# Performance work log

Measured on AMD Instinct MI355X. Metric: run time of the kernel, lower is better.

Reference implementation:

```python
import jax, jax.numpy as jnp
import numpy as np

N = 100000   # nodes
E = 1600000  # edges (avg degree 16)
D = 128      # feature / hidden dim
C = 64       # classes
L = 4        # number of GCNII layers
ALPHA = 0.1
LAMDA = 0.5


def setup_inputs() -> dict:
    key = jax.random.key(0)
    ks = jax.random.split(key, 8)
    stdv = 1.0 / np.sqrt(D)
    x = jax.random.normal(ks[0], (N, D), jnp.float32)
    edge_src = jax.random.randint(ks[1], (E,), 0, N)
    edge_dst = jax.random.randint(ks[2], (E,), 0, N)
    edge_weight = jax.random.uniform(ks[3], (E,), jnp.float32)
    w_in = jax.random.uniform(ks[4], (D, D), jnp.float32, -stdv, stdv)
    b_in = jnp.zeros((D,), jnp.float32)
    gcn_w = jax.random.uniform(ks[5], (L, D, D), jnp.float32, -stdv, stdv)
    w_out = jax.random.uniform(ks[6], (D, C), jnp.float32, -stdv, stdv)
    b_out = jnp.zeros((C,), jnp.float32)
    return {"x": x, "edge_src": edge_src, "edge_dst": edge_dst,
            "edge_weight": edge_weight, "w_in": w_in, "b_in": b_in,
            "gcn_w": gcn_w, "w_out": w_out, "b_out": b_out}


def _spmm(edge_src, edge_dst, edge_weight, h):
    # torch.sparse.mm(adj, h): out[i] = sum_j adj[i,j] * h[j]
    # row = dst, col = src in COO terms.
    return jax.ops.segment_sum(edge_weight[:, None] * h[edge_src],
                               edge_dst, num_segments=N)


def reference(x, edge_src, edge_dst, edge_weight, w_in, b_in, gcn_w, w_out, b_out):
    h0 = jax.nn.relu(x @ w_in + b_in)          # [N, D] initial residual
    h = h0
    for l in range(L):
        # GCNConvII called with l_arg = l+1 -> theta = log(lamda/(l_arg+1) + 1)
        theta = float(np.log(LAMDA / (l + 2) + 1.0))
        hi = _spmm(edge_src, edge_dst, edge_weight, h)      # sparse SpMM
        support = (1.0 - ALPHA) * hi + ALPHA * h0           # initial-residual mix
        out = theta * (support @ gcn_w[l]) + (1.0 - theta) * support
        out = out + h                                       # identity residual
        h = jax.nn.relu(out)
    logits = h @ w_out + b_out                              # [N, C]
    return jax.nn.log_softmax(logits, axis=1)
```

## Files before the change

### kernel.cpp

```cpp
#include <hip/hip_runtime.h>
#include <hip/hip_fp16.h>
#include <math.h>

#define N_NODES 100000
#define N_EDGES 1600000
#define DIM     128
#define NCLS    64
#define ALPHA   0.1f

#define NB      391
#define CAP     5120
#define NF      ((size_t)N_NODES * DIM)
#define STRIPES (N_NODES / 16)
#define CHUNK   4096

typedef __attribute__((ext_vector_type(8))) _Float16 f16x8;
typedef __attribute__((ext_vector_type(4))) float    f32x4;

__device__ __forceinline__ __half2 u2h2(unsigned int u) {
    union { unsigned int u; __half2 h; } x; x.u = u; return x.h;
}
__device__ __forceinline__ unsigned int h22u(__half2 h) {
    union { unsigned int u; __half2 h; } x; x.h = h; return x.u;
}


__global__ __launch_bounds__(256) void k_part(const int* __restrict__ src,
                                              const int* __restrict__ dst,
                                              const float* __restrict__ ew,
                                              int* __restrict__ bucket_cursor,
                                              int2* __restrict__ ebuf) {
    __shared__ int lhist[NB], gbase[NB];
    int t = threadIdx.x;
    for (int b = t; b < NB; b += 256) lhist[b] = 0;
    __syncthreads();
    int base = blockIdx.x * CHUNK;
    int end = min(base + CHUNK, N_EDGES);
    for (int i = base + t; i < end; i += 256)
        atomicAdd(&lhist[dst[i] >> 8], 1);
    __syncthreads();
    for (int b = t; b < NB; b += 256) {
        int c = lhist[b];
        gbase[b] = c ? atomicAdd(&bucket_cursor[b], c) : 0;
        lhist[b] = 0;
    }
    __syncthreads();
    for (int i = base + t; i < end; i += 256) {
        int d = dst[i];
        int b = d >> 8;
        int r = atomicAdd(&lhist[b], 1);
        ebuf[(size_t)b * CAP + gbase[b] + r] =
            make_int2(src[i] | ((d & 255) << 17),
                      __float_as_int((1.0f - ALPHA) * ew[i]));
    }
}

__global__ __launch_bounds__(256) void k_sortbucket(
    const int2* __restrict__ ebuf, const int* __restrict__ bucket_cursor,
    int2* __restrict__ rowspan, int2* __restrict__ colw) {
    __shared__ int cnt[256], pref[256], lcur[256];
    int t = threadIdx.x, b = blockIdx.x;
    cnt[t] = 0;
    __syncthreads();
    int beg = b * CAP, end = beg + bucket_cursor[b];
    for (int i = beg + t; i < end; i += 256)
        atomicAdd(&cnt[ebuf[i].x >> 17], 1);
    __syncthreads();
    int v = cnt[t];
    pref[t] = v;
    __syncthreads();
    for (int off = 1; off < 256; off <<= 1) {
        int u = (t >= off) ? pref[t - off] : 0;
        __syncthreads();
        pref[t] += u;
        __syncthreads();
    }
    int excl = pref[t] - v;
    int node = b * 256 + t;
    if (node < N_NODES) rowspan[node] = make_int2(beg + excl, beg + excl + v);
    lcur[t] = beg + excl;
    __syncthreads();
    for (int i = beg + t; i < end; i += 256) {
        int2 e = ebuf[i];
        int pos = atomicAdd(&lcur[e.x >> 17], 1);
        unsigned int w2 = h22u(__float2half2_rn(__int_as_float(e.y)));
        colw[pos] = make_int2(e.x & 0x1FFFF, (int)w2);
    }
}

__global__ void k_prepw(const float* __restrict__ gcnw, const float* __restrict__ wout,
                        const float* __restrict__ win, unsigned short* __restrict__ wp,
                        int* __restrict__ bucket_cursor) {
    int tid = blockIdx.x * 256 + threadIdx.x;
    if (tid < NB) bucket_cursor[tid] = 0;
    if (tid < 65536) {
        int l = tid >> 14;
        int r = tid & 16383;
        int j = r & 7, lane = (r >> 3) & 63, ch = (r >> 9) & 3, nt = r >> 11;
        int n = nt * 16 + (lane & 15);
        int k = ch * 32 + (lane >> 4) * 8 + j;
        float theta = logf(0.5f / (float)(l + 2) + 1.0f);
        float v = theta * gcnw[l * 16384 + k * 128 + n] + ((k == n) ? (1.f - theta) : 0.f);
        wp[tid] = __half_as_ushort(__float2half(v));
    } else if (tid < 73728) {
        int r = tid - 65536;
        int j = r & 7, lane = (r >> 3) & 63, ch = (r >> 9) & 3, nt = r >> 11;
        int n = nt * 16 + (lane & 15);
        int k = ch * 32 + (lane >> 4) * 8 + j;
        wp[tid] = __half_as_ushort(__float2half(wout[k * 64 + n]));
    } else if (tid < 90112) {
        int r = tid - 73728;
        int j = r & 7, lane = (r >> 3) & 63, ch = (r >> 9) & 3, nt = r >> 11;
        int n = nt * 16 + (lane & 15);
        int k = ch * 32 + (lane >> 4) * 8 + j;
        wp[tid] = __half_as_ushort(__float2half(win[k * 128 + n]));
    }
}

__device__ __forceinline__ void gather_tile(
    const int2* __restrict__ rowspan, const int2* __restrict__ colw,
    const unsigned short* __restrict__ h, const unsigned short* __restrict__ h0,
    unsigned short* sup, int r0, int wave, int slot, int seg) {
    __half2 z2 = __float2half2_rn(0.f);
    __half2 al2 = __float2half2_rn(ALPHA);
    for (int i = 0; i < 4; i++) {
        int n_loc = wave * 4 + i;
        int node = r0 + n_loc;
        int2 span = rowspan[node];
        int beg = span.x, end = span.y;

        __half2 acc2[4] = {z2, z2, z2, z2};
        if (slot == 0) {
            uint4 z = *(const uint4*)(h0 + (size_t)node * DIM + seg * 8);
            acc2[0] = __hmul2(al2, u2h2(z.x));
            acc2[1] = __hmul2(al2, u2h2(z.y));
            acc2[2] = __hmul2(al2, u2h2(z.z));
            acc2[3] = __hmul2(al2, u2h2(z.w));
        }

        int last = end - 1;
        for (int e = beg; e < end; e += 16) {
            int e0 = e + slot, e1 = e0 + 4, e2 = e0 + 8, e3 = e0 + 12;
            int2 c0 = colw[min(e0, last)];
            int2 c1 = colw[min(e1, last)];
            int2 c2 = colw[min(e2, last)];
            int2 c3 = colw[min(e3, last)];
            uint4 r0v = *(const uint4*)(h + (size_t)c0.x * DIM + seg * 8);
            uint4 r1v = *(const uint4*)(h + (size_t)c1.x * DIM + seg * 8);
            uint4 r2v = *(const uint4*)(h + (size_t)c2.x * DIM + seg * 8);
            uint4 r3v = *(const uint4*)(h + (size_t)c3.x * DIM + seg * 8);
            __half2 w0 = (e0 < end) ? u2h2((unsigned int)c0.y) : z2;
            __half2 w1 = (e1 < end) ? u2h2((unsigned int)c1.y) : z2;
            __half2 w2 = (e2 < end) ? u2h2((unsigned int)c2.y) : z2;
            __half2 w3 = (e3 < end) ? u2h2((unsigned int)c3.y) : z2;
            acc2[0] = __hfma2(w0, u2h2(r0v.x), acc2[0]);
            acc2[1] = __hfma2(w0, u2h2(r0v.y), acc2[1]);
            acc2[2] = __hfma2(w0, u2h2(r0v.z), acc2[2]);
            acc2[3] = __hfma2(w0, u2h2(r0v.w), acc2[3]);
            acc2[0] = __hfma2(w1, u2h2(r1v.x), acc2[0]);
            acc2[1] = __hfma2(w1, u2h2(r1v.y), acc2[1]);
            acc2[2] = __hfma2(w1, u2h2(r1v.z), acc2[2]);
            acc2[3] = __hfma2(w1, u2h2(r1v.w), acc2[3]);
            acc2[0] = __hfma2(w2, u2h2(r2v.x), acc2[0]);
            acc2[1] = __hfma2(w2, u2h2(r2v.y), acc2[1]);
            acc2[2] = __hfma2(w2, u2h2(r2v.z), acc2[2]);
            acc2[3] = __hfma2(w2, u2h2(r2v.w), acc2[3]);
            acc2[0] = __hfma2(w3, u2h2(r3v.x), acc2[0]);
            acc2[1] = __hfma2(w3, u2h2(r3v.y), acc2[1]);
            acc2[2] = __hfma2(w3, u2h2(r3v.z), acc2[2]);
            acc2[3] = __hfma2(w3, u2h2(r3v.w), acc2[3]);
        }

        #pragma unroll
        for (int j = 0; j < 4; j++) {
            unsigned int u = __shfl_xor(h22u(acc2[j]), 16);
            acc2[j] = __hadd2(acc2[j], u2h2(u));
            u = __shfl_xor(h22u(acc2[j]), 32);
            acc2[j] = __hadd2(acc2[j], u2h2(u));
        }

        if (slot == 0) {
            int g = seg ^ n_loc;
            *(uint4*)(sup + n_loc * 128 + g * 8) =
                make_uint4(h22u(acc2[0]), h22u(acc2[1]), h22u(acc2[2]), h22u(acc2[3]));
        }
    }
}

__global__ __launch_bounds__(256, 6) void k_layer_fused(
    const int2* __restrict__ rowspan, const int2* __restrict__ colw,
    const unsigned short* __restrict__ h,
    const unsigned short* __restrict__ h0,
    const unsigned short* __restrict__ wp,
    unsigned short* __restrict__ hout) {
    __shared__ unsigned short sup[16 * 128];
    int wave = threadIdx.x >> 6, lane = threadIdx.x & 63;
    int slot = lane >> 4, seg = lane & 15;
    int r0 = blockIdx.x * 16;

    gather_tile(rowspan, colw, h, h0, sup, r0, wave, slot, seg);
    __syncthreads();

    int m = lane & 15, q = lane >> 4;
    f32x4 acc[2];
    acc[0] = (f32x4){0.f, 0.f, 0.f, 0.f};
    acc[1] = (f32x4){0.f, 0.f, 0.f, 0.f};
    #pragma unroll
    for (int ch = 0; ch < 4; ch++) {
        int g = (4 * ch + q) ^ m;
        f16x8 a = *(const f16x8*)(sup + m * 128 + g * 8);
        #pragma unroll
        for (int t2 = 0; t2 < 2; t2++) {
            int nt = wave * 2 + t2;
            f16x8 b = *(const f16x8*)(wp + (((nt * 4 + ch) * 64 + lane) << 3));
            acc[t2] = __builtin_amdgcn_mfma_f32_16x16x32_f16(a, b, acc[t2], 0, 0, 0);
        }
    }
    #pragma unroll
    for (int t2 = 0; t2 < 2; t2++) {
        int col = (wave * 2 + t2) * 16 + m;
        #pragma unroll
        for (int r = 0; r < 4; r++) {
            int row = r0 + q * 4 + r;
            size_t idx = (size_t)row * DIM + col;
            float hp = __half2float(__ushort_as_half(h[idx]));
            float o = acc[t2][r] + hp;
            hout[idx] = __half_as_ushort(__float2half(fmaxf(o, 0.f)));
        }
    }
}

__global__ __launch_bounds__(256, 6) void k_layer_fused_out(
    const int2* __restrict__ rowspan, const int2* __restrict__ colw,
    const unsigned short* __restrict__ h, const unsigned short* __restrict__ h0,
    const unsigned short* __restrict__ wp,
    const unsigned short* __restrict__ wpo,
    const float* __restrict__ bo, float* __restrict__ out) {
    __shared__ unsigned short sup[16 * 128];
    __shared__ unsigned short hfin[16 * 128];
    int wave = threadIdx.x >> 6, lane = threadIdx.x & 63;
    int slot = lane >> 4, seg = lane & 15;
    int r0 = blockIdx.x * 16;

    gather_tile(rowspan, colw, h, h0, sup, r0, wave, slot, seg);
    __syncthreads();

    int m = lane & 15, q = lane >> 4;
    f32x4 acc[2];
    acc[0] = (f32x4){0.f, 0.f, 0.f, 0.f};
    acc[1] = (f32x4){0.f, 0.f, 0.f, 0.f};
    #pragma unroll
    for (int ch = 0; ch < 4; ch++) {
        int g = (4 * ch + q) ^ m;
        f16x8 a = *(const f16x8*)(sup + m * 128 + g * 8);
        #pragma unroll
        for (int t2 = 0; t2 < 2; t2++) {
            int nt = wave * 2 + t2;
            f16x8 b = *(const f16x8*)(wp + (((nt * 4 + ch) * 64 + lane) << 3));
            acc[t2] = __builtin_amdgcn_mfma_f32_16x16x32_f16(a, b, acc[t2], 0, 0, 0);
        }
    }
    #pragma unroll
    for (int t2 = 0; t2 < 2; t2++) {
        int col = (wave * 2 + t2) * 16 + m;
        #pragma unroll
        for (int r = 0; r < 4; r++) {
            int row = q * 4 + r;
            size_t idx = (size_t)(r0 + row) * DIM + col;
            float hp = __half2float(__ushort_as_half(h[idx]));
            float o = fmaxf(acc[t2][r] + hp, 0.f);
            hfin[row * 128 + ((col >> 3) ^ row) * 8 + (col & 7)] =
                __half_as_ushort(__float2half(o));
        }
    }
    __syncthreads();

    if (wave == 0) {
        f32x4 acc4[4];
        #pragma unroll
        for (int nt = 0; nt < 4; nt++) acc4[nt] = (f32x4){0.f, 0.f, 0.f, 0.f};
        #pragma unroll
        for (int ch = 0; ch < 4; ch++) {
            int g = (4 * ch + q) ^ m;
            f16x8 a = *(const f16x8*)(hfin + m * 128 + g * 8);
            #pragma unroll
            for (int nt = 0; nt < 4; nt++) {
                f16x8 b = *(const f16x8*)(wpo + (((nt * 4 + ch) * 64 + lane) << 3));
                acc4[nt] = __builtin_amdgcn_mfma_f32_16x16x32_f16(a, b, acc4[nt], 0, 0, 0);
            }
        }
        float v[4][4];
        #pragma unroll
        for (int nt = 0; nt < 4; nt++) {
            float bias = bo[nt * 16 + m];
            #pragma unroll
            for (int r = 0; r < 4; r++) v[nt][r] = acc4[nt][r] + bias;
        }
        #pragma unroll
        for (int r = 0; r < 4; r++) {
            float mx = fmaxf(fmaxf(v[0][r], v[1][r]), fmaxf(v[2][r], v[3][r]));
            #pragma unroll
            for (int off = 1; off < 16; off <<= 1) mx = fmaxf(mx, __shfl_xor(mx, off));
            float s = 0.f;
            #pragma unroll
            for (int nt = 0; nt < 4; nt++) s += __expf(v[nt][r] - mx);
            #pragma unroll
            for (int off = 1; off < 16; off <<= 1) s += __shfl_xor(s, off);
            float lse = mx + logf(s);
            int row = r0 + q * 4 + r;
            #pragma unroll
            for (int nt = 0; nt < 4; nt++)
                out[(size_t)row * NCLS + nt * 16 + m] = v[nt][r] - lse;
        }
    }
}

__global__ __launch_bounds__(256) void k_in_mfma(
    const float* __restrict__ x, const unsigned short* __restrict__ wp,
    const float* __restrict__ b_in, unsigned short* __restrict__ h0) {
    int wave = threadIdx.x >> 6, lane = threadIdx.x & 63;
    int stripe = blockIdx.x * 4 + wave;
    if (stripe >= STRIPES) return;
    int r0 = stripe * 16;
    int m = lane & 15, q = lane >> 4;

    f32x4 acc[8];
    #pragma unroll
    for (int nt = 0; nt < 8; nt++) acc[nt] = (f32x4){0.f, 0.f, 0.f, 0.f};

    const float* xr = x + (size_t)(r0 + m) * DIM + q * 8;
    #pragma unroll
    for (int ch = 0; ch < 4; ch++) {
        float4 a0 = *(const float4*)(xr + ch * 32);
        float4 a1 = *(const float4*)(xr + ch * 32 + 4);
        f16x8 a;
        a[0] = (_Float16)a0.x; a[1] = (_Float16)a0.y;
        a[2] = (_Float16)a0.z; a[3] = (_Float16)a0.w;
        a[4] = (_Float16)a1.x; a[5] = (_Float16)a1.y;
        a[6] = (_Float16)a1.z; a[7] = (_Float16)a1.w;
        #pragma unroll
        for (int nt = 0; nt < 8; nt++) {
            f16x8 b = *(const f16x8*)(wp + (((nt * 4 + ch) * 64 + lane) << 3));
            acc[nt] = __builtin_amdgcn_mfma_f32_16x16x32_f16(a, b, acc[nt], 0, 0, 0);
        }
    }

    #pragma unroll
    for (int nt = 0; nt < 8; nt++) {
        int col = nt * 16 + m;
        float bias = b_in[col];
        #pragma unroll
        for (int r = 0; r < 4; r++) {
            int row = r0 + q * 4 + r;
            h0[(size_t)row * DIM + col] =
                __half_as_ushort(__float2half(fmaxf(acc[nt][r] + bias, 0.f)));
        }
    }
}

extern "C" void kernel_launch(void* const* d_in, const int* in_sizes, int n_in,
                              void* d_out, int out_size, void* d_ws, size_t ws_size,
                              hipStream_t stream) {
    const float* x    = (const float*)d_in[0];
    const int*   esrc = (const int*)d_in[1];
    const int*   edst = (const int*)d_in[2];
    const float* ew   = (const float*)d_in[3];
    const float* w_in = (const float*)d_in[4];
    const float* b_in = (const float*)d_in[5];
    const float* gcnw = (const float*)d_in[6];
    const float* wout = (const float*)d_in[7];
    const float* bout = (const float*)d_in[8];
    float* out = (float*)d_out;

    unsigned short* h0 = (unsigned short*)d_ws;
    unsigned short* hA = h0 + NF;
    unsigned short* hB = hA + NF;
    unsigned short* wp = hB + NF;
    int2* colw = (int2*)(wp + 90112);
    int2* ebuf = colw + (size_t)NB * CAP;
    int2* rowspan = ebuf + (size_t)NB * CAP;
    int*  bucket_cursor = (int*)(rowspan + N_NODES);

    const int PART_B = (N_EDGES + CHUNK - 1) / CHUNK;
    const int MFMA_BLOCKS = (STRIPES + 3) / 4;

    k_prepw<<<(90112 + 255) / 256, 256, 0, stream>>>(gcnw, wout, w_in, wp,
                                                     bucket_cursor);

    k_part<<<PART_B, 256, 0, stream>>>(esrc, edst, ew, bucket_cursor, ebuf);
    k_sortbucket<<<NB, 256, 0, stream>>>(ebuf, bucket_cursor, rowspan, colw);

    k_in_mfma<<<MFMA_BLOCKS, 256, 0, stream>>>(x, wp + 73728, b_in, h0);

    const unsigned short* hprev = h0;
    unsigned short* bufs[2] = {hA, hB};
    for (int l = 0; l < 3; l++) {
        unsigned short* hnew = bufs[l & 1];
        k_layer_fused<<<STRIPES, 256, 0, stream>>>(rowspan, colw, hprev, h0,
                                                   wp + (size_t)l * 16384, hnew);
        hprev = hnew;
    }
    k_layer_fused_out<<<STRIPES, 256, 0, stream>>>(rowspan, colw, hprev, h0,
                                                   wp + 3 * 16384, wp + 65536,
                                                   bout, out);
}
```

Baseline: 461.2 us.

## Gather neighbor features from FP8 copies with fp32 accumulation in SpMM

Each layer now writes an extra FP8 (e4m3) copy of its output, and the input projection writes one for h0. The SpMM gather reads these 8-byte-per-segment rows instead of 16-byte fp16 rows, which halves the random-gather traffic that dominates each layer. Accumulation moves from packed fp16 to fp32, and edge weights stay fp32 in colw. The cost is extra FP8 writes, an additional LDS transpose with barriers, and a large loss of precision in the aggregated features that may exceed tolerance. CAP is also shrunk, and the h0 FP8 buffer reuses the edge staging area.

```diff
diff --git a/kernel.cpp b/kernel.cpp
--- a/kernel.cpp
+++ b/kernel.cpp
@@ -9,19 +9,21 @@
 #define ALPHA   0.1f
 
 #define NB      391
-#define CAP     5120
+#define CAP     4608
 #define NF      ((size_t)N_NODES * DIM)
 #define STRIPES (N_NODES / 16)
 #define CHUNK   4096
 
 typedef __attribute__((ext_vector_type(8))) _Float16 f16x8;
 typedef __attribute__((ext_vector_type(4))) float    f32x4;
+typedef __attribute__((ext_vector_type(2))) float    f32x2;
 
 __device__ __forceinline__ __half2 u2h2(unsigned int u) {
     union { unsigned int u; __half2 h; } x; x.u = u; return x.h;
 }
-__device__ __forceinline__ unsigned int h22u(__half2 h) {
-    union { unsigned int u; __half2 h; } x; x.h = h; return x.u;
+__device__ __forceinline__ unsigned int pkrtz(float a, float b) {
+    auto h = __builtin_amdgcn_cvt_pkrtz(a, b);
+    union { decltype(h) v; unsigned int u; } x; x.v = h; return x.u;
 }
 
 
@@ -83,8 +85,7 @@
     for (int i = beg + t; i < end; i += 256) {
         int2 e = ebuf[i];
         int pos = atomicAdd(&lcur[e.x >> 17], 1);
-        unsigned int w2 = h22u(__float2half2_rn(__int_as_float(e.y)));
-        colw[pos] = make_int2(e.x & 0x1FFFF, (int)w2);
+        colw[pos] = make_int2(e.x & 0x1FFFF, e.y);
     }
 }
 
@@ -117,25 +118,27 @@
     }
 }
 
-__device__ __forceinline__ void gather_tile(
+__device__ __forceinline__ void gather_tile8(
     const int2* __restrict__ rowspan, const int2* __restrict__ colw,
-    const unsigned short* __restrict__ h, const unsigned short* __restrict__ h0,
+    const unsigned char* __restrict__ h8, const unsigned short* __restrict__ h0,
     unsigned short* sup, int r0, int wave, int slot, int seg) {
-    __half2 z2 = __float2half2_rn(0.f);
-    __half2 al2 = __float2half2_rn(ALPHA);
     for (int i = 0; i < 4; i++) {
         int n_loc = wave * 4 + i;
         int node = r0 + n_loc;
         int2 span = rowspan[node];
         int beg = span.x, end = span.y;
 
-        __half2 acc2[4] = {z2, z2, z2, z2};
+        float acc[8] = {0.f, 0.f, 0.f, 0.f, 0.f, 0.f, 0.f, 0.f};
         if (slot == 0) {
             uint4 z = *(const uint4*)(h0 + (size_t)node * DIM + seg * 8);
-            acc2[0] = __hmul2(al2, u2h2(z.x));
-            acc2[1] = __hmul2(al2, u2h2(z.y));
-            acc2[2] = __hmul2(al2, u2h2(z.z));
-            acc2[3] = __hmul2(al2, u2h2(z.w));
+            float2 f0 = __half22float2(u2h2(z.x));
+            float2 f1 = __half22float2(u2h2(z.y));
+            float2 f2 = __half22float2(u2h2(z.z));
+            float2 f3 = __half22float2(u2h2(z.w));
+            acc[0] = ALPHA * f0.x; acc[1] = ALPHA * f0.y;
+            acc[2] = ALPHA * f1.x; acc[3] = ALPHA * f1.y;
+            acc[4] = ALPHA * f2.x; acc[5] = ALPHA * f2.y;
+            acc[6] = ALPHA * f3.x; acc[7] = ALPHA * f3.y;
         }
 
         int last = end - 1;
@@ -145,60 +148,62 @@
             int2 c1 = colw[min(e1, last)];
             int2 c2 = colw[min(e2, last)];
             int2 c3 = colw[min(e3, last)];
-            uint4 r0v = *(const uint4*)(h + (size_t)c0.x * DIM + seg * 8);
-            uint4 r1v = *(const uint4*)(h + (size_t)c1.x * DIM + seg * 8);
-            uint4 r2v = *(const uint4*)(h + (size_t)c2.x * DIM + seg * 8);
-            uint4 r3v = *(const uint4*)(h + (size_t)c3.x * DIM + seg * 8);
-            __half2 w0 = (e0 < end) ? u2h2((unsigned int)c0.y) : z2;
-            __half2 w1 = (e1 < end) ? u2h2((unsigned int)c1.y) : z2;
-            __half2 w2 = (e2 < end) ? u2h2((unsigned int)c2.y) : z2;
-            __half2 w3 = (e3 < end) ? u2h2((unsigned int)c3.y) : z2;
-            acc2[0] = __hfma2(w0, u2h2(r0v.x), acc2[0]);
-            acc2[1] = __hfma2(w0, u2h2(r0v.y), acc2[1]);
-            acc2[2] = __hfma2(w0, u2h2(r0v.z), acc2[2]);
-            acc2[3] = __hfma2(w0, u2h2(r0v.w), acc2[3]);
-            acc2[0] = __hfma2(w1, u2h2(r1v.x), acc2[0]);
-            acc2[1] = __hfma2(w1, u2h2(r1v.y), acc2[1]);
-            acc2[2] = __hfma2(w1, u2h2(r1v.z), acc2[2]);
-            acc2[3] = __hfma2(w1, u2h2(r1v.w), acc2[3]);
-            acc2[0] = __hfma2(w2, u2h2(r2v.x), acc2[0]);
-            acc2[1] = __hfma2(w2, u2h2(r2v.y), acc2[1]);
-            acc2[2] = __hfma2(w2, u2h2(r2v.z), acc2[2]);
-            acc2[3] = __hfma2(w2, u2h2(r2v.w), acc2[3]);
-            acc2[0] = __hfma2(w3, u2h2(r3v.x), acc2[0]);
-            acc2[1] = __hfma2(w3, u2h2(r3v.y), acc2[1]);
-            acc2[2] = __hfma2(w3, u2h2(r3v.z), acc2[2]);
-            acc2[3] = __hfma2(w3, u2h2(r3v.w), acc2[3]);
-        }
-
-        #pragma unroll
-        for (int j = 0; j < 4; j++) {
-            unsigned int u = __shfl_xor(h22u(acc2[j]), 16);
-            acc2[j] = __hadd2(acc2[j], u2h2(u));
-            u = __shfl_xor(h22u(acc2[j]), 32);
-            acc2[j] = __hadd2(acc2[j], u2h2(u));
+            uint2 r0v = *(const uint2*)(h8 + (size_t)c0.x * DIM + seg * 8);
+            uint2 r1v = *(const uint2*)(h8 + (size_t)c1.x * DIM + seg * 8);
+            uint2 r2v = *(const uint2*)(h8 + (size_t)c2.x * DIM + seg * 8);
+            uint2 r3v = *(const uint2*)(h8 + (size_t)c3.x * DIM + seg * 8);
+            float w0 = (e0 < end) ? __int_as_float(c0.y) : 0.f;
+            float w1 = (e1 < end) ? __int_as_float(c1.y) : 0.f;
+            float w2 = (e2 < end) ? __int_as_float(c2.y) : 0.f;
+            float w3 = (e3 < end) ? __int_as_float(c3.y) : 0.f;
+            f32x2 p;
+            p = __builtin_amdgcn_cvt_pk_f32_fp8(r0v.x, false); acc[0] += w0 * p.x; acc[1] += w0 * p.y;
+            p = __builtin_amdgcn_cvt_pk_f32_fp8(r0v.x, true);  acc[2] += w0 * p.x; acc[3] += w0 * p.y;
+            p = __builtin_amdgcn_cvt_pk_f32_fp8(r0v.y, false); acc[4] += w0 * p.x; acc[5] += w0 * p.y;
+            p = __builtin_amdgcn_cvt_pk_f32_fp8(r0v.y, true);  acc[6] += w0 * p.x; acc[7] += w0 * p.y;
+            p = __builtin_amdgcn_cvt_pk_f32_fp8(r1v.x, false); acc[0] += w1 * p.x; acc[1] += w1 * p.y;
+            p = __builtin_amdgcn_cvt_pk_f32_fp8(r1v.x, true);  acc[2] += w1 * p.x; acc[3] += w1 * p.y;
+            p = __builtin_amdgcn_cvt_pk_f32_fp8(r1v.y, false); acc[4] += w1 * p.x; acc[5] += w1 * p.y;
+            p = __builtin_amdgcn_cvt_pk_f32_fp8(r1v.y, true);  acc[6] += w1 * p.x; acc[7] += w1 * p.y;
+            p = __builtin_amdgcn_cvt_pk_f32_fp8(r2v.x, false); acc[0] += w2 * p.x; acc[1] += w2 * p.y;
+            p = __builtin_amdgcn_cvt_pk_f32_fp8(r2v.x, true);  acc[2] += w2 * p.x; acc[3] += w2 * p.y;
+            p = __builtin_amdgcn_cvt_pk_f32_fp8(r2v.y, false); acc[4] += w2 * p.x; acc[5] += w2 * p.y;
+            p = __builtin_amdgcn_cvt_pk_f32_fp8(r2v.y, true);  acc[6] += w2 * p.x; acc[7] += w2 * p.y;
+            p = __builtin_amdgcn_cvt_pk_f32_fp8(r3v.x, false); acc[0] += w3 * p.x; acc[1] += w3 * p.y;
+            p = __builtin_amdgcn_cvt_pk_f32_fp8(r3v.x, true);  acc[2] += w3 * p.x; acc[3] += w3 * p.y;
+            p = __builtin_amdgcn_cvt_pk_f32_fp8(r3v.y, false); acc[4] += w3 * p.x; acc[5] += w3 * p.y;
+            p = __builtin_amdgcn_cvt_pk_f32_fp8(r3v.y, true);  acc[6] += w3 * p.x; acc[7] += w3 * p.y;
+        }
+
+        #pragma unroll
+        for (int j = 0; j < 8; j++) {
+            acc[j] += __shfl_xor(acc[j], 16);
+            acc[j] += __shfl_xor(acc[j], 32);
         }
 
         if (slot == 0) {
             int g = seg ^ n_loc;
             *(uint4*)(sup + n_loc * 128 + g * 8) =
-                make_uint4(h22u(acc2[0]), h22u(acc2[1]), h22u(acc2[2]), h22u(acc2[3]));
+                make_uint4(pkrtz(acc[0], acc[1]), pkrtz(acc[2], acc[3]),
+                           pkrtz(acc[4], acc[5]), pkrtz(acc[6], acc[7]));
         }
     }
 }
 
 __global__ __launch_bounds__(256, 6) void k_layer_fused(
     const int2* __restrict__ rowspan, const int2* __restrict__ colw,
+    const unsigned char* __restrict__ h8src,
     const unsigned short* __restrict__ h,
     const unsigned short* __restrict__ h0,
     const unsigned short* __restrict__ wp,
-    unsigned short* __restrict__ hout) {
+    unsigned short* __restrict__ hout,
+    unsigned char* __restrict__ hout8) {
     __shared__ unsigned short sup[16 * 128];
     int wave = threadIdx.x >> 6, lane = threadIdx.x & 63;
     int slot = lane >> 4, seg = lane & 15;
     int r0 = blockIdx.x * 16;
 
-    gather_tile(rowspan, colw, h, h0, sup, r0, wave, slot, seg);
+    gather_tile8(rowspan, colw, h8src, h0, sup, r0, wave, slot, seg);
     __syncthreads();
 
     int m = lane & 15, q = lane >> 4;
@@ -216,6 +221,7 @@
             acc[t2] = __builtin_amdgcn_mfma_f32_16x16x32_f16(a, b, acc[t2], 0, 0, 0);
         }
     }
+    float ov[2][4];
     #pragma unroll
     for (int t2 = 0; t2 < 2; t2++) {
         int col = (wave * 2 + t2) * 16 + m;
@@ -224,14 +230,37 @@
             int row = r0 + q * 4 + r;
             size_t idx = (size_t)row * DIM + col;
             float hp = __half2float(__ushort_as_half(h[idx]));
-            float o = acc[t2][r] + hp;
-            hout[idx] = __half_as_ushort(__float2half(fmaxf(o, 0.f)));
-        }
+            float o = fmaxf(acc[t2][r] + hp, 0.f);
+            ov[t2][r] = o;
+            hout[idx] = __half_as_ushort(__float2half(o));
+        }
+    }
+    if (hout8 != nullptr) {
+        __syncthreads();
+        unsigned char* s8 = (unsigned char*)sup;
+        #pragma unroll
+        for (int t2 = 0; t2 < 2; t2++) {
+            int col = (wave * 2 + t2) * 16 + m;
+            #pragma unroll
+            for (int rp = 0; rp < 2; rp++) {
+                unsigned int pk = __builtin_amdgcn_cvt_pk_fp8_f32(
+                    ov[t2][2 * rp], ov[t2][2 * rp + 1], 0, false);
+                int row0 = q * 4 + 2 * rp;
+                s8[row0 * 128 + col] = (unsigned char)(pk & 0xFF);
+                s8[(row0 + 1) * 128 + col] = (unsigned char)((pk >> 8) & 0xFF);
+            }
+        }
+        __syncthreads();
+        int t = threadIdx.x;
+        int row = t >> 4, sg = t & 15;
+        *(uint2*)(hout8 + (size_t)(r0 + row) * DIM + sg * 8) =
+            *(const uint2*)(s8 + row * 128 + sg * 8);
     }
 }
 
 __global__ __launch_bounds__(256, 6) void k_layer_fused_out(
     const int2* __restrict__ rowspan, const int2* __restrict__ colw,
+    const unsigned char* __restrict__ h8src,
     const unsigned short* __restrict__ h, const unsigned short* __restrict__ h0,
     const unsigned short* __restrict__ wp,
     const unsigned short* __restrict__ wpo,
@@ -242,7 +271,7 @@
     int slot = lane >> 4, seg = lane & 15;
     int r0 = blockIdx.x * 16;
 
-    gather_tile(rowspan, colw, h, h0, sup, r0, wave, slot, seg);
+    gather_tile8(rowspan, colw, h8src, h0, sup, r0, wave, slot, seg);
     __syncthreads();
 
     int m = lane & 15, q = lane >> 4;
@@ -317,7 +346,8 @@
 
 __global__ __launch_bounds__(256) void k_in_mfma(
     const float* __restrict__ x, const unsigned short* __restrict__ wp,
-    const float* __restrict__ b_in, unsigned short* __restrict__ h0) {
+    const float* __restrict__ b_in, unsigned short* __restrict__ h0,
+    unsigned char* __restrict__ h08) {
     int wave = threadIdx.x >> 6, lane = threadIdx.x & 63;
     int stripe = blockIdx.x * 4 + wave;
     if (stripe >= STRIPES) return;
@@ -349,11 +379,21 @@
     for (int nt = 0; nt < 8; nt++) {
         int col = nt * 16 + m;
         float bias = b_in[col];
+        float o4[4];
         #pragma unroll
         for (int r = 0; r < 4; r++) {
             int row = r0 + q * 4 + r;
-            h0[(size_t)row * DIM + col] =
-                __half_as_ushort(__float2half(fmaxf(acc[nt][r] + bias, 0.f)));
+            float o = fmaxf(acc[nt][r] + bias, 0.f);
+            o4[r] = o;
+            h0[(size_t)row * DIM + col] = __half_as_ushort(__float2half(o));
+        }
+        #pragma unroll
+        for (int rp = 0; rp < 2; rp++) {
+            unsigned int pk = __builtin_amdgcn_cvt_pk_fp8_f32(
+                o4[2 * rp], o4[2 * rp + 1], 0, false);
+            int row0 = r0 + q * 4 + 2 * rp;
+            h08[(size_t)row0 * DIM + col] = (unsigned char)(pk & 0xFF);
+            h08[(size_t)(row0 + 1) * DIM + col] = (unsigned char)((pk >> 8) & 0xFF);
         }
     }
 }
@@ -380,6 +420,9 @@
     int2* ebuf = colw + (size_t)NB * CAP;
     int2* rowspan = ebuf + (size_t)NB * CAP;
     int*  bucket_cursor = (int*)(rowspan + N_NODES);
+    unsigned char* hA8 = (unsigned char*)(bucket_cursor + NB);
+    unsigned char* hB8 = hA8 + NF;
+    unsigned char* h08 = (unsigned char*)ebuf;
 
     const int PART_B = (N_EDGES + CHUNK - 1) / CHUNK;
     const int MFMA_BLOCKS = (STRIPES + 3) / 4;
@@ -390,17 +433,15 @@
     k_part<<<PART_B, 256, 0, stream>>>(esrc, edst, ew, bucket_cursor, ebuf);
     k_sortbucket<<<NB, 256, 0, stream>>>(ebuf, bucket_cursor, rowspan, colw);
 
-    k_in_mfma<<<MFMA_BLOCKS, 256, 0, stream>>>(x, wp + 73728, b_in, h0);
-
-    const unsigned short* hprev = h0;
-    unsigned short* bufs[2] = {hA, hB};
-    for (int l = 0; l < 3; l++) {
-        unsigned short* hnew = bufs[l & 1];
-        k_layer_fused<<<STRIPES, 256, 0, stream>>>(rowspan, colw, hprev, h0,
-                                                   wp + (size_t)l * 16384, hnew);
-        hprev = hnew;
-    }
-    k_layer_fused_out<<<STRIPES, 256, 0, stream>>>(rowspan, colw, hprev, h0,
+    k_in_mfma<<<MFMA_BLOCKS, 256, 0, stream>>>(x, wp + 73728, b_in, h0, h08);
+
+    k_layer_fused<<<STRIPES, 256, 0, stream>>>(rowspan, colw, h08, h0, h0,
+                                               wp + 0 * 16384, hA, hA8);
+    k_layer_fused<<<STRIPES, 256, 0, stream>>>(rowspan, colw, hA8, hA, h0,
+                                               wp + 1 * 16384, hB, hB8);
+    k_layer_fused<<<STRIPES, 256, 0, stream>>>(rowspan, colw, hB8, hB, h0,
+                                               wp + 2 * 16384, hA, hA8);
+    k_layer_fused_out<<<STRIPES, 256, 0, stream>>>(rowspan, colw, hA8, hA, h0,
                                                    wp + 3 * 16384, wp + 65536,
                                                    bout, out);
 }
```

After: 454.8 us. About the same (-1.4%).
